# Kernel tuning notes

Measured on AMD Instinct MI355X. Metric: run time of the kernel, lower is better.

The kernel has to match this reference:

```python
import jax, jax.numpy as jnp
import numpy as np

HEADS = 4
DIM_HEAD = 128


def setup_inputs() -> dict:
    key = jax.random.key(0)
    k1, k2, k3, k4 = jax.random.split(key, 4)
    B, C, H, W = 8, 256, 64, 64
    hidden = HEADS * DIM_HEAD  # 512
    x = jax.random.normal(k1, (B, C, H, W), dtype=jnp.float32)
    # 1x1 convs are just channel matmuls; store kernels as [out_ch, in_ch]
    w_qkv = jax.random.normal(k2, (3 * hidden, C), dtype=jnp.float32) * 0.05
    w_out = jax.random.normal(k3, (C, hidden), dtype=jnp.float32) * 0.05
    b_out = jax.random.normal(k4, (C,), dtype=jnp.float32) * 0.05
    return {"x": x, "w_qkv": w_qkv, "w_out": w_out, "b_out": b_out}


def reference(x, w_qkv, w_out, b_out):
    B, C, H, W = x.shape
    n = H * W
    # to_qkv: 1x1 conv without bias == channel matmul
    qkv = jnp.einsum('bchw,oc->bohw', x, w_qkv)  # [B, 3*heads*dim_head, H, W]
    qkv = qkv.reshape(B, 3, HEADS, DIM_HEAD, n)  # 'b (qkv heads c) h w -> b qkv heads c n'
    q, k, v = qkv[:, 0], qkv[:, 1], qkv[:, 2]    # each [B, heads, dim_head, n]
    k = jax.nn.softmax(k, axis=-1)               # softmax over spatial positions
    context = jnp.einsum('bhdn,bhen->bhde', k, v)   # [B, heads, d, e]
    out = jnp.einsum('bhde,bhdn->bhen', context, q)  # [B, heads, e, n]
    out = out.reshape(B, HEADS * DIM_HEAD, H, W)
    # to_out: 1x1 conv with bias
    return jnp.einsum('bchw,oc->bohw', out, w_out) + b_out[None, :, None, None]
```

## Files before the change

kernel.cpp:

```cpp
#include <hip/hip_runtime.h>
#include <stdint.h>


using frag8 = __attribute__((ext_vector_type(8))) short;
using f32x4 = __attribute__((ext_vector_type(4))) float;

__device__ __forceinline__ float bf2f(unsigned short u) {
    union { unsigned int u; float f; } c;
    c.u = ((unsigned int)u) << 16;
    return c.f;
}
__device__ __forceinline__ unsigned short f2bf(float f) {
    union { float f; unsigned int u; } c; c.f = f;
    unsigned int u = c.u;
    return (unsigned short)((u + 0x7FFFu + ((u >> 16) & 1u)) >> 16);
}

__device__ __forceinline__ void gl_lds16(const void* g, void* l) {
    __builtin_amdgcn_global_load_lds(
        (const __attribute__((address_space(1))) unsigned int*)g,
        (__attribute__((address_space(3))) unsigned int*)l, 16, 0, 0);
}

__global__ __launch_bounds__(256) void k0_weights(
    const float* __restrict__ w_qkv, const float* __restrict__ w_out,
    unsigned short* __restrict__ wkb, unsigned short* __restrict__ woutb,
    unsigned short* __restrict__ wqT, unsigned short* __restrict__ wvT)
{
    __shared__ float T[64][65];
    const int blk = blockIdx.x;
    const int tid = threadIdx.x;
    if (blk < 128) {
        const int idx = (blk * 256 + tid) * 4;
        float4 v = *(const float4*)(w_qkv + 512 * 256 + idx);
        ushort4 o;
        o.x = f2bf(v.x); o.y = f2bf(v.y); o.z = f2bf(v.z); o.w = f2bf(v.w);
        *(ushort4*)(wkb + idx) = o;
    } else if (blk < 256) {
        const int idx = ((blk - 128) * 256 + tid) * 4;
        float4 v = *(const float4*)(w_out + idx);
        ushort4 o;
        o.x = f2bf(v.x); o.y = f2bf(v.y); o.z = f2bf(v.z); o.w = f2bf(v.w);
        *(ushort4*)(woutb + idx) = o;
    } else {
        const int t2 = blk - 256;
        const int which = t2 >> 5;
        const int t = t2 & 31;
        const int j0 = (t >> 2) * 64, c0 = (t & 3) * 64;
        const float* src = w_qkv + (which ? 1024 * 256 : 0);
        unsigned short* dst = which ? wvT : wqT;
        const int r = tid >> 4, cc = (tid & 15) * 4;
        #pragma unroll
        for (int p = 0; p < 4; ++p) {
            float4 v = *(const float4*)(src + (j0 + r + p * 16) * 256 + c0 + cc);
            T[r + p * 16][cc + 0] = v.x; T[r + p * 16][cc + 1] = v.y;
            T[r + p * 16][cc + 2] = v.z; T[r + p * 16][cc + 3] = v.w;
        }
        __syncthreads();
        const int c = tid >> 2, jj = (tid & 3) * 16;
        #pragma unroll
        for (int g = 0; g < 4; ++g) {
            ushort4 o;
            o.x = f2bf(T[jj + g * 4 + 0][c]);
            o.y = f2bf(T[jj + g * 4 + 1][c]);
            o.z = f2bf(T[jj + g * 4 + 2][c]);
            o.w = f2bf(T[jj + g * 4 + 3][c]);
            *(ushort4*)(dst + (c0 + c) * 512 + j0 + jj + g * 4) = o;
        }
    }
}

__global__ __launch_bounds__(256) void k0_xt(
    const float* __restrict__ x, unsigned short* __restrict__ xbT,
    unsigned short* __restrict__ xbc)
{
    __shared__ float T[64][65];
    const int tid = threadIdx.x;
    const int n0 = blockIdx.x * 64, c0 = blockIdx.y * 64, b = blockIdx.z;
    const float* xb = x + (size_t)b * 1048576;
    const int cr = tid >> 4, nc = (tid & 15) * 4;
    #pragma unroll
    for (int p = 0; p < 4; ++p) {
        float4 v = *(const float4*)(xb + (size_t)(c0 + cr + p * 16) * 4096 + n0 + nc);
        T[cr + p * 16][nc + 0] = v.x; T[cr + p * 16][nc + 1] = v.y;
        T[cr + p * 16][nc + 2] = v.z; T[cr + p * 16][nc + 3] = v.w;
        ushort4 o;
        o.x = f2bf(v.x); o.y = f2bf(v.y); o.z = f2bf(v.z); o.w = f2bf(v.w);
        *(ushort4*)(xbc + (size_t)b * 1048576 + (size_t)(c0 + cr + p * 16) * 4096 + n0 + nc) = o;
    }
    __syncthreads();
    const int n = tid >> 2, cc = (tid & 3) * 16;
    unsigned short* dst = xbT + (size_t)b * 1048576 + (size_t)(n0 + n) * 256 + c0 + cc;
    #pragma unroll
    for (int g = 0; g < 4; ++g) {
        ushort4 o;
        o.x = f2bf(T[cc + g * 4 + 0][n]);
        o.y = f2bf(T[cc + g * 4 + 1][n]);
        o.z = f2bf(T[cc + g * 4 + 2][n]);
        o.w = f2bf(T[cc + g * 4 + 3][n]);
        *(ushort4*)(dst + g * 4) = o;
    }
}

template<int MODE>
__global__ __launch_bounds__(256) void mfma_bt(
    const unsigned short* __restrict__ A0, int lda,
    const unsigned short* __restrict__ B0, int ldb,
    void* __restrict__ C0, int ldc,
    const float* __restrict__ bias, int Kp,
    unsigned long long sAz, unsigned long long sBz, unsigned long long sCz)
{
    __shared__ unsigned short As[128 * 32];
    __shared__ unsigned short Bs[128 * 32];
    const int tid  = threadIdx.x;
    const int w    = tid >> 6, lane = tid & 63;
    const int quad = lane >> 4, l16 = lane & 15;
    const int wm = (w >> 1) * 64, wn = (w & 1) * 64;
    const int z = blockIdx.z;

    const unsigned short* A;
    const unsigned short* B;
    int ks, ke, m0, n0;
    if constexpr (MODE == 3) {
        m0 = blockIdx.y * 128; n0 = 0;
        ks = 0; ke = 256;
        A = A0 + (unsigned long long)(z & 3) * 65536ull + (unsigned long long)m0 * lda;
        B = B0 + (unsigned long long)(z >> 2) * 131072ull + (unsigned long long)(z & 3) * 32768ull;
    } else if constexpr (MODE == 4) {
        m0 = blockIdx.y * 128; n0 = (blockIdx.x & 1) * 128;
        ks = (blockIdx.x >> 1) * 1024; ke = ks + 1024;
        A = A0 + sAz * z + (unsigned long long)m0 * lda;
        B = B0 + sBz * z + (unsigned long long)n0 * ldb;
    } else {
        m0 = blockIdx.y * 128; n0 = blockIdx.x * 128;
        ks = 0; ke = Kp;
        A = A0 + sAz * z + (unsigned long long)m0 * lda;
        B = B0 + sBz * z + (unsigned long long)n0 * ldb;
    }

    const int cA0 = w * 128 + lane;
    const int cA1 = cA0 + 64;
    const unsigned short* gA0 = A + (unsigned long long)(cA0 >> 2) * lda + (cA0 & 3) * 8;
    const unsigned short* gA1 = A + (unsigned long long)(cA1 >> 2) * lda + (cA1 & 3) * 8;
    const unsigned short* gB0 = B + (unsigned long long)(cA0 >> 2) * ldb + (cA0 & 3) * 8;
    const unsigned short* gB1 = B + (unsigned long long)(cA1 >> 2) * ldb + (cA1 & 3) * 8;
    unsigned short* lA0 = As + w * 1024;
    unsigned short* lA1 = As + w * 1024 + 512;
    unsigned short* lB0 = Bs + w * 1024;
    unsigned short* lB1 = Bs + w * 1024 + 512;

    f32x4 acc[4][4] = {};

    for (int k0 = ks; k0 < ke; k0 += 32) {
        gl_lds16(gA0 + k0, lA0);
        gl_lds16(gA1 + k0, lA1);
        gl_lds16(gB0 + k0, lB0);
        gl_lds16(gB1 + k0, lB1);
        __syncthreads();
        frag8 a[4], b[4];
        #pragma unroll
        for (int t = 0; t < 4; ++t) {
            a[t] = *(const frag8*)(As + (wm + t * 16 + l16) * 32 + quad * 8);
            b[t] = *(const frag8*)(Bs + (wn + t * 16 + l16) * 32 + quad * 8);
        }
        #pragma unroll
        for (int mt = 0; mt < 4; ++mt)
            #pragma unroll
            for (int nt = 0; nt < 4; ++nt)
                acc[mt][nt] = __builtin_amdgcn_mfma_f32_16x16x32_bf16(
                    a[mt], b[nt], acc[mt][nt], 0, 0, 0);
        __syncthreads();
    }

    if constexpr (MODE == 0 || MODE == 3) {
        unsigned short* C;
        if constexpr (MODE == 0)
            C = (unsigned short*)C0 + sCz * z + (unsigned long long)m0 * ldc + n0;
        else
            C = (unsigned short*)C0 + (unsigned long long)(z >> 2) * 131072ull
              + (unsigned long long)(z & 3) * 128ull + (unsigned long long)m0 * ldc;
        #pragma unroll
        for (int mt = 0; mt < 4; ++mt) {
            const int row = wm + mt * 16 + quad * 4;
            #pragma unroll
            for (int nt = 0; nt < 4; ++nt) {
                const int col = wn + nt * 16 + l16;
                #pragma unroll
                for (int r = 0; r < 4; ++r)
                    C[(unsigned long long)(row + r) * ldc + col] = f2bf(acc[mt][nt][r]);
            }
        }
    } else if constexpr (MODE == 1) {
        float* C = (float*)C0 + sCz * z + (unsigned long long)m0 * ldc + n0;
        const float* bp = bias + m0;
        #pragma unroll
        for (int mt = 0; mt < 4; ++mt) {
            const int row = wm + mt * 16 + quad * 4;
            #pragma unroll
            for (int nt = 0; nt < 4; ++nt) {
                const int col = wn + nt * 16 + l16;
                #pragma unroll
                for (int r = 0; r < 4; ++r)
                    C[(unsigned long long)(row + r) * ldc + col] = acc[mt][nt][r] + bp[row + r];
            }
        }
    } else {
        float* C = (float*)C0 + (unsigned long long)(blockIdx.x >> 1) * 1048576ull
                 + sCz * z + (unsigned long long)m0 * ldc + n0;
        #pragma unroll
        for (int mt = 0; mt < 4; ++mt) {
            const int row = wm + mt * 16 + quad * 4;
            #pragma unroll
            for (int nt = 0; nt < 4; ++nt) {
                const int col = wn + nt * 16 + l16;
                #pragma unroll
                for (int r = 0; r < 4; ++r)
                    C[(unsigned long long)(row + r) * ldc + col] = acc[mt][nt][r];
            }
        }
    }
}

__global__ __launch_bounds__(256) void k2_softmax(unsigned short* __restrict__ Kb)
{
    __shared__ float red[4];
    unsigned short* row = Kb + (size_t)blockIdx.x * 4096;
    const int tid = threadIdx.x;
    float v[16];
    #pragma unroll
    for (int g = 0; g < 4; ++g) {
        ushort4 u = *(const ushort4*)(row + g * 1024 + tid * 4);
        v[g * 4 + 0] = bf2f(u.x); v[g * 4 + 1] = bf2f(u.y);
        v[g * 4 + 2] = bf2f(u.z); v[g * 4 + 3] = bf2f(u.w);
    }
    float m = -1e30f;
    #pragma unroll
    for (int i = 0; i < 16; ++i) m = fmaxf(m, v[i]);
    #pragma unroll
    for (int off = 32; off > 0; off >>= 1) m = fmaxf(m, __shfl_down(m, off, 64));
    if ((tid & 63) == 0) red[tid >> 6] = m;
    __syncthreads();
    m = fmaxf(fmaxf(red[0], red[1]), fmaxf(red[2], red[3]));
    __syncthreads();
    float s = 0.f;
    #pragma unroll
    for (int i = 0; i < 16; ++i) { v[i] = __expf(v[i] - m); s += v[i]; }
    #pragma unroll
    for (int off = 32; off > 0; off >>= 1) s += __shfl_down(s, off, 64);
    if ((tid & 63) == 0) red[tid >> 6] = s;
    __syncthreads();
    s = red[0] + red[1] + red[2] + red[3];
    const float inv = 1.0f / s;
    #pragma unroll
    for (int g = 0; g < 4; ++g) {
        ushort4 u;
        u.x = f2bf(v[g * 4 + 0] * inv); u.y = f2bf(v[g * 4 + 1] * inv);
        u.z = f2bf(v[g * 4 + 2] * inv); u.w = f2bf(v[g * 4 + 3] * inv);
        *(ushort4*)(row + g * 1024 + tid * 4) = u;
    }
}

__global__ __launch_bounds__(256) void k3_sum(
    const float* __restrict__ Gp, unsigned short* __restrict__ G)
{
    const int idx = (blockIdx.x * 256 + threadIdx.x) * 4;
    float4 s = make_float4(0.f, 0.f, 0.f, 0.f);
    #pragma unroll
    for (int sl = 0; sl < 4; ++sl) {
        float4 t = *(const float4*)(Gp + (size_t)sl * 1048576 + idx);
        s.x += t.x; s.y += t.y; s.z += t.z; s.w += t.w;
    }
    ushort4 o;
    o.x = f2bf(s.x); o.y = f2bf(s.y); o.z = f2bf(s.z); o.w = f2bf(s.w);
    *(ushort4*)(G + idx) = o;
}

extern "C" void kernel_launch(void* const* d_in, const int* in_sizes, int n_in,
                              void* d_out, int out_size, void* d_ws, size_t ws_size,
                              hipStream_t stream) {
    (void)in_sizes; (void)n_in; (void)out_size; (void)ws_size;
    const float* x     = (const float*)d_in[0];
    const float* w_qkv = (const float*)d_in[1];
    const float* w_out = (const float*)d_in[2];
    const float* b_out = (const float*)d_in[3];
    float* out = (float*)d_out;

    char* ws = (char*)d_ws;
    unsigned short* Kb    = (unsigned short*)ws;
    unsigned short* xbT   = (unsigned short*)(ws + 33554432);
    unsigned short* xbc   = (unsigned short*)(ws + 50331648);
    unsigned short* wkb   = (unsigned short*)(ws + 67108864);
    unsigned short* woutb = (unsigned short*)(ws + 67371008);
    unsigned short* wqT   = (unsigned short*)(ws + 67633152);
    unsigned short* wvT   = (unsigned short*)(ws + 67895296);
    unsigned short* U     = (unsigned short*)(ws + 68157440);
    float*          Gp    = (float*)(ws + 68681728);
    unsigned short* G     = (unsigned short*)(ws + 85458944);
    unsigned short* Mb    = (unsigned short*)(ws + 87556096);
    unsigned short* Nb    = (unsigned short*)(ws + 89653248);

    k0_weights<<<dim3(320), 256, 0, stream>>>(w_qkv, w_out, wkb, woutb, wqT, wvT);
    mfma_bt<0><<<dim3(2, 2, 4), 256, 0, stream>>>(
        woutb, 512, wvT, 512, U, 256, nullptr, 128,
        128ull, 128ull, 65536ull);
    k0_xt<<<dim3(64, 4, 8), 256, 0, stream>>>(x, xbT, xbc);
    mfma_bt<0><<<dim3(32, 4, 8), 256, 0, stream>>>(
        wkb, 256, xbT, 256, Kb, 4096, nullptr, 256,
        0ull, 1048576ull, 2097152ull);
    k2_softmax<<<dim3(4096), 256, 0, stream>>>(Kb);
    mfma_bt<4><<<dim3(8, 4, 8), 256, 0, stream>>>(
        Kb, 4096, xbc, 4096, Gp, 256, nullptr, 0,
        2097152ull, 1048576ull, 131072ull);
    k3_sum<<<dim3(1024), 256, 0, stream>>>(Gp, G);
    mfma_bt<3><<<dim3(1, 2, 32), 256, 0, stream>>>(
        U, 256, G, 256, Mb, 512, nullptr, 256,
        0ull, 0ull, 0ull);
    mfma_bt<0><<<dim3(2, 2, 8), 256, 0, stream>>>(
        Mb, 512, wqT, 512, Nb, 256, nullptr, 512,
        131072ull, 0ull, 65536ull);
    mfma_bt<1><<<dim3(32, 2, 8), 256, 0, stream>>>(
        Nb, 256, xbT, 256, out, 4096, b_out, 256,
        65536ull, 1048576ull, 1048576ull);
}
```

Baseline: 194.5 us.

## Fuse key softmax into K projection epilogue and defer normalization to context sum

The K-projection GEMM epilogue now writes exp(k) directly in bf16 and accumulates row sums through atomics. The separate softmax kernel is removed, and the division by the row sum moves into the k3_sum reduction of the context. The U = W_out·W_v precompute is folded into the weight-prep kernel as a small fp32 SIMT GEMM, which drops one launch and the bf16 conversions of w_out and w_v. Skipping max subtraction risks overflow for large logits, and the atomics add contention.

```diff
diff --git a/kernel.cpp b/kernel.cpp
--- a/kernel.cpp
+++ b/kernel.cpp
@@ -24,8 +24,8 @@
 
 __global__ __launch_bounds__(256) void k0_weights(
     const float* __restrict__ w_qkv, const float* __restrict__ w_out,
-    unsigned short* __restrict__ wkb, unsigned short* __restrict__ woutb,
-    unsigned short* __restrict__ wqT, unsigned short* __restrict__ wvT)
+    unsigned short* __restrict__ wkb, unsigned short* __restrict__ wqT,
+    unsigned short* __restrict__ U, float* __restrict__ rs)
 {
     __shared__ float T[64][65];
     const int blk = blockIdx.x;
@@ -36,23 +36,13 @@
         ushort4 o;
         o.x = f2bf(v.x); o.y = f2bf(v.y); o.z = f2bf(v.z); o.w = f2bf(v.w);
         *(ushort4*)(wkb + idx) = o;
-    } else if (blk < 256) {
-        const int idx = ((blk - 128) * 256 + tid) * 4;
-        float4 v = *(const float4*)(w_out + idx);
-        ushort4 o;
-        o.x = f2bf(v.x); o.y = f2bf(v.y); o.z = f2bf(v.z); o.w = f2bf(v.w);
-        *(ushort4*)(woutb + idx) = o;
-    } else {
-        const int t2 = blk - 256;
-        const int which = t2 >> 5;
-        const int t = t2 & 31;
+    } else if (blk < 160) {
+        const int t = blk - 128;
         const int j0 = (t >> 2) * 64, c0 = (t & 3) * 64;
-        const float* src = w_qkv + (which ? 1024 * 256 : 0);
-        unsigned short* dst = which ? wvT : wqT;
         const int r = tid >> 4, cc = (tid & 15) * 4;
         #pragma unroll
         for (int p = 0; p < 4; ++p) {
-            float4 v = *(const float4*)(src + (j0 + r + p * 16) * 256 + c0 + cc);
+            float4 v = *(const float4*)(w_qkv + (j0 + r + p * 16) * 256 + c0 + cc);
             T[r + p * 16][cc + 0] = v.x; T[r + p * 16][cc + 1] = v.y;
             T[r + p * 16][cc + 2] = v.z; T[r + p * 16][cc + 3] = v.w;
         }
@@ -65,8 +55,50 @@
             o.y = f2bf(T[jj + g * 4 + 1][c]);
             o.z = f2bf(T[jj + g * 4 + 2][c]);
             o.w = f2bf(T[jj + g * 4 + 3][c]);
-            *(ushort4*)(dst + (c0 + c) * 512 + j0 + jj + g * 4) = o;
-        }
+            *(ushort4*)(wqT + (c0 + c) * 512 + j0 + jj + g * 4) = o;
+        }
+    } else if (blk < 224) {
+        float (*As)[65] = &T[0];
+        float (*Bs)[65] = &T[16];
+        const int ub = blk - 160;
+        const int h = ub >> 4, rem = ub & 15;
+        const int o0 = (rem >> 2) * 64, c0 = (rem & 3) * 64;
+        const int tm = tid >> 4, tn = tid & 15;
+        const int ar = tid >> 2, ac = (tid & 3) * 4;
+        const int br = tid >> 4, bc = (tid & 15) * 4;
+        float acc[4][4] = {};
+        for (int e0 = 0; e0 < 128; e0 += 16) {
+            float4 a4 = *(const float4*)(w_out + (o0 + ar) * 512 + h * 128 + e0 + ac);
+            float4 b4 = *(const float4*)(w_qkv + (1024 + h * 128 + e0 + br) * 256 + c0 + bc);
+            __syncthreads();
+            As[ac + 0][ar] = a4.x; As[ac + 1][ar] = a4.y;
+            As[ac + 2][ar] = a4.z; As[ac + 3][ar] = a4.w;
+            Bs[br][bc + 0] = b4.x; Bs[br][bc + 1] = b4.y;
+            Bs[br][bc + 2] = b4.z; Bs[br][bc + 3] = b4.w;
+            __syncthreads();
+            #pragma unroll
+            for (int kk = 0; kk < 16; ++kk) {
+                float a[4], bb[4];
+                #pragma unroll
+                for (int i = 0; i < 4; ++i) a[i] = As[kk][tm * 4 + i];
+                #pragma unroll
+                for (int j = 0; j < 4; ++j) bb[j] = Bs[kk][tn * 4 + j];
+                #pragma unroll
+                for (int i = 0; i < 4; ++i)
+                    #pragma unroll
+                    for (int j = 0; j < 4; ++j) acc[i][j] += a[i] * bb[j];
+            }
+        }
+        #pragma unroll
+        for (int i = 0; i < 4; ++i) {
+            ushort4 o;
+            o.x = f2bf(acc[i][0]); o.y = f2bf(acc[i][1]);
+            o.z = f2bf(acc[i][2]); o.w = f2bf(acc[i][3]);
+            *(ushort4*)(U + h * 65536 + (o0 + tm * 4 + i) * 256 + c0 + tn * 4) = o;
+        }
+    } else {
+        const int idx = ((blk - 224) * 256 + tid) * 4;
+        *(float4*)(rs + idx) = make_float4(0.f, 0.f, 0.f, 0.f);
     }
 }
 
@@ -108,7 +140,8 @@
     const unsigned short* __restrict__ B0, int ldb,
     void* __restrict__ C0, int ldc,
     const float* __restrict__ bias, int Kp,
-    unsigned long long sAz, unsigned long long sBz, unsigned long long sCz)
+    unsigned long long sAz, unsigned long long sBz, unsigned long long sCz,
+    float* __restrict__ aux)
 {
     __shared__ unsigned short As[128 * 32];
     __shared__ unsigned short Bs[128 * 32];
@@ -204,7 +237,7 @@
                     C[(unsigned long long)(row + r) * ldc + col] = acc[mt][nt][r] + bp[row + r];
             }
         }
-    } else {
+    } else if constexpr (MODE == 4) {
         float* C = (float*)C0 + (unsigned long long)(blockIdx.x >> 1) * 1048576ull
                  + sCz * z + (unsigned long long)m0 * ldc + n0;
         #pragma unroll
@@ -218,52 +251,48 @@
                     C[(unsigned long long)(row + r) * ldc + col] = acc[mt][nt][r];
             }
         }
-    }
-}
-
-__global__ __launch_bounds__(256) void k2_softmax(unsigned short* __restrict__ Kb)
-{
-    __shared__ float red[4];
-    unsigned short* row = Kb + (size_t)blockIdx.x * 4096;
-    const int tid = threadIdx.x;
-    float v[16];
-    #pragma unroll
-    for (int g = 0; g < 4; ++g) {
-        ushort4 u = *(const ushort4*)(row + g * 1024 + tid * 4);
-        v[g * 4 + 0] = bf2f(u.x); v[g * 4 + 1] = bf2f(u.y);
-        v[g * 4 + 2] = bf2f(u.z); v[g * 4 + 3] = bf2f(u.w);
-    }
-    float m = -1e30f;
-    #pragma unroll
-    for (int i = 0; i < 16; ++i) m = fmaxf(m, v[i]);
-    #pragma unroll
-    for (int off = 32; off > 0; off >>= 1) m = fmaxf(m, __shfl_down(m, off, 64));
-    if ((tid & 63) == 0) red[tid >> 6] = m;
-    __syncthreads();
-    m = fmaxf(fmaxf(red[0], red[1]), fmaxf(red[2], red[3]));
-    __syncthreads();
-    float s = 0.f;
-    #pragma unroll
-    for (int i = 0; i < 16; ++i) { v[i] = __expf(v[i] - m); s += v[i]; }
-    #pragma unroll
-    for (int off = 32; off > 0; off >>= 1) s += __shfl_down(s, off, 64);
-    if ((tid & 63) == 0) red[tid >> 6] = s;
-    __syncthreads();
-    s = red[0] + red[1] + red[2] + red[3];
-    const float inv = 1.0f / s;
-    #pragma unroll
-    for (int g = 0; g < 4; ++g) {
-        ushort4 u;
-        u.x = f2bf(v[g * 4 + 0] * inv); u.y = f2bf(v[g * 4 + 1] * inv);
-        u.z = f2bf(v[g * 4 + 2] * inv); u.w = f2bf(v[g * 4 + 3] * inv);
-        *(ushort4*)(row + g * 1024 + tid * 4) = u;
+    } else {
+        unsigned short* C = (unsigned short*)C0 + sCz * z
+                          + (unsigned long long)m0 * ldc + n0;
+        float rp[4][4] = {};
+        #pragma unroll
+        for (int mt = 0; mt < 4; ++mt) {
+            const int row = wm + mt * 16 + quad * 4;
+            #pragma unroll
+            for (int nt = 0; nt < 4; ++nt) {
+                const int col = wn + nt * 16 + l16;
+                #pragma unroll
+                for (int r = 0; r < 4; ++r) {
+                    const float e = __expf(acc[mt][nt][r]);
+                    C[(unsigned long long)(row + r) * ldc + col] = f2bf(e);
+                    rp[mt][r] += e;
+                }
+            }
+        }
+        #pragma unroll
+        for (int m = 1; m < 16; m <<= 1)
+            #pragma unroll
+            for (int mt = 0; mt < 4; ++mt)
+                #pragma unroll
+                for (int r = 0; r < 4; ++r)
+                    rp[mt][r] += __shfl_xor(rp[mt][r], m, 64);
+        if (l16 == 0) {
+            float* rsb = aux + z * 512 + m0;
+            #pragma unroll
+            for (int mt = 0; mt < 4; ++mt)
+                #pragma unroll
+                for (int r = 0; r < 4; ++r)
+                    atomicAdd(rsb + wm + mt * 16 + quad * 4 + r, rp[mt][r]);
+        }
     }
 }
 
 __global__ __launch_bounds__(256) void k3_sum(
-    const float* __restrict__ Gp, unsigned short* __restrict__ G)
+    const float* __restrict__ Gp, const float* __restrict__ rs,
+    unsigned short* __restrict__ G)
 {
     const int idx = (blockIdx.x * 256 + threadIdx.x) * 4;
+    const float inv = 1.0f / rs[idx >> 8];
     float4 s = make_float4(0.f, 0.f, 0.f, 0.f);
     #pragma unroll
     for (int sl = 0; sl < 4; ++sl) {
@@ -271,7 +300,8 @@
         s.x += t.x; s.y += t.y; s.z += t.z; s.w += t.w;
     }
     ushort4 o;
-    o.x = f2bf(s.x); o.y = f2bf(s.y); o.z = f2bf(s.z); o.w = f2bf(s.w);
+    o.x = f2bf(s.x * inv); o.y = f2bf(s.y * inv);
+    o.z = f2bf(s.z * inv); o.w = f2bf(s.w * inv);
     *(ushort4*)(G + idx) = o;
 }
 
@@ -286,39 +316,34 @@
     float* out = (float*)d_out;
 
     char* ws = (char*)d_ws;
-    unsigned short* Kb    = (unsigned short*)ws;
-    unsigned short* xbT   = (unsigned short*)(ws + 33554432);
-    unsigned short* xbc   = (unsigned short*)(ws + 50331648);
-    unsigned short* wkb   = (unsigned short*)(ws + 67108864);
-    unsigned short* woutb = (unsigned short*)(ws + 67371008);
-    unsigned short* wqT   = (unsigned short*)(ws + 67633152);
-    unsigned short* wvT   = (unsigned short*)(ws + 67895296);
-    unsigned short* U     = (unsigned short*)(ws + 68157440);
-    float*          Gp    = (float*)(ws + 68681728);
-    unsigned short* G     = (unsigned short*)(ws + 85458944);
-    unsigned short* Mb    = (unsigned short*)(ws + 87556096);
-    unsigned short* Nb    = (unsigned short*)(ws + 89653248);
-
-    k0_weights<<<dim3(320), 256, 0, stream>>>(w_qkv, w_out, wkb, woutb, wqT, wvT);
-    mfma_bt<0><<<dim3(2, 2, 4), 256, 0, stream>>>(
-        woutb, 512, wvT, 512, U, 256, nullptr, 128,
-        128ull, 128ull, 65536ull);
+    unsigned short* Kexp = (unsigned short*)ws;
+    unsigned short* xbT  = (unsigned short*)(ws + 33554432);
+    unsigned short* xbc  = (unsigned short*)(ws + 50331648);
+    unsigned short* wkb  = (unsigned short*)(ws + 67108864);
+    unsigned short* wqT  = (unsigned short*)(ws + 67371008);
+    unsigned short* U    = (unsigned short*)(ws + 67633152);
+    float*          rs   = (float*)(ws + 68157440);
+    float*          Gp   = (float*)(ws + 68173824);
+    unsigned short* G    = (unsigned short*)(ws + 84951040);
+    unsigned short* Mb   = (unsigned short*)(ws + 87048192);
+    unsigned short* Nb   = (unsigned short*)(ws + 89145344);
+
+    k0_weights<<<dim3(228), 256, 0, stream>>>(w_qkv, w_out, wkb, wqT, U, rs);
     k0_xt<<<dim3(64, 4, 8), 256, 0, stream>>>(x, xbT, xbc);
-    mfma_bt<0><<<dim3(32, 4, 8), 256, 0, stream>>>(
-        wkb, 256, xbT, 256, Kb, 4096, nullptr, 256,
-        0ull, 1048576ull, 2097152ull);
-    k2_softmax<<<dim3(4096), 256, 0, stream>>>(Kb);
+    mfma_bt<5><<<dim3(32, 4, 8), 256, 0, stream>>>(
+        wkb, 256, xbT, 256, Kexp, 4096, nullptr, 256,
+        0ull, 1048576ull, 2097152ull, rs);
     mfma_bt<4><<<dim3(8, 4, 8), 256, 0, stream>>>(
-        Kb, 4096, xbc, 4096, Gp, 256, nullptr, 0,
-        2097152ull, 1048576ull, 131072ull);
-    k3_sum<<<dim3(1024), 256, 0, stream>>>(Gp, G);
+        Kexp, 4096, xbc, 4096, Gp, 256, nullptr, 0,
+        2097152ull, 1048576ull, 131072ull, nullptr);
+    k3_sum<<<dim3(1024), 256, 0, stream>>>(Gp, rs, G);
     mfma_bt<3><<<dim3(1, 2, 32), 256, 0, stream>>>(
         U, 256, G, 256, Mb, 512, nullptr, 256,
-        0ull, 0ull, 0ull);
+        0ull, 0ull, 0ull, nullptr);
     mfma_bt<0><<<dim3(2, 2, 8), 256, 0, stream>>>(
         Mb, 512, wqT, 512, Nb, 256, nullptr, 512,
-        131072ull, 0ull, 65536ull);
+        131072ull, 0ull, 65536ull, nullptr);
     mfma_bt<1><<<dim3(32, 2, 8), 256, 0, stream>>>(
         Nb, 256, xbT, 256, out, 4096, b_out, 256,
-        65536ull, 1048576ull, 1048576ull);
-}
+        65536ull, 1048576ull, 1048576ull, nullptr);
+}
```

Result: slower. 201.5 us (+3.6%).
